# Kernel optimization log

Hardware: AMD Instinct MI355X
Metric: run time of the kernel (lower is better)

## Reference

```python
import jax, jax.numpy as jnp
import numpy as np

N_NODES = 20000
N_EDGES = 100000
WALK_LEN = 4
FEAT_DIM = 256
HID = 64
NUM_HEAD = 8
H_RNN = NUM_HEAD * HID  # 512
OUT_DIM = 16


def setup_inputs() -> dict:
    key = jax.random.key(0)
    ks = jax.random.split(key, 12)
    s = 0.05  # small init scale for numerical stability
    return {
        "x": jax.random.normal(ks[0], (N_NODES, FEAT_DIM), jnp.float32),
        "W_mlp": jax.random.normal(ks[1], (HID, FEAT_DIM), jnp.float32) * s,
        "b_mlp": jnp.zeros((HID,), jnp.float32),
        "W_ih": jax.random.normal(ks[2], (3 * H_RNN, HID), jnp.float32) * s,
        "W_hh": jax.random.normal(ks[3], (3 * H_RNN, H_RNN), jnp.float32) * s,
        "b_ih": jnp.zeros((3 * H_RNN,), jnp.float32),
        "b_hh": jnp.zeros((3 * H_RNN,), jnp.float32),
        "attn": jax.random.normal(ks[4], (1, NUM_HEAD, HID), jnp.float32) * s,
        "W_emb": jax.random.normal(ks[5], (HID, H_RNN), jnp.float32) * s,
        "b_emb": jnp.zeros((HID,), jnp.float32),
        "W_last": jax.random.normal(ks[6], (OUT_DIM, HID), jnp.float32) * s,
        "b_last": jnp.zeros((OUT_DIM,), jnp.float32),
        "edge_metapath_indices": jax.random.randint(ks[7], (N_EDGES, WALK_LEN), 0, N_NODES),
        "num_nodes": N_NODES,
    }


def reference(x, W_mlp, b_mlp, W_ih, W_hh, b_ih, b_hh, attn, W_emb, b_emb,
              W_last, b_last, edge_metapath_indices, num_nodes):
    # self channel: embedding = mlp(data.x)
    emb = x @ W_mlp.T + b_mlp                       # [N, hid]

    # rnn channel: gather per-metapath node embeddings
    edata = emb[edge_metapath_indices]              # [E, L, hid]
    E = edata.shape[0]
    h_rnn = W_hh.shape[1]

    # torch nn.GRU cell (gate order r, z, n), scan over path length
    def gru_step(h, x_t):
        xg = x_t @ W_ih.T + b_ih                    # [E, 3H]
        hg = h @ W_hh.T + b_hh                      # [E, 3H]
        xr, xz, xn = jnp.split(xg, 3, axis=-1)
        hr, hz, hn = jnp.split(hg, 3, axis=-1)
        r = jax.nn.sigmoid(xr + hr)
        z = jax.nn.sigmoid(xz + hz)
        n = jnp.tanh(xn + r * hn)
        return (1.0 - z) * n + z * h, None

    h0 = jnp.zeros((E, h_rnn), edata.dtype)
    hT, _ = jax.lax.scan(gru_step, h0, jnp.swapaxes(edata, 0, 1))  # [E, 8*hid]

    num_head, hid = attn.shape[1], attn.shape[2]
    eft = hT.reshape(E, num_head, hid)              # per-edge features

    # attention logits + leaky_relu(0.01)
    a = jnp.sum(eft * attn, axis=-1)                # [E, num_head]
    a = jnp.where(a > 0, a, 0.01 * a)

    # edge softmax grouped by destination node (indices[:, -1])
    dst = edge_metapath_indices[:, -1]
    m = jax.ops.segment_max(a, dst, num_segments=num_nodes)        # [N, H]
    ea = jnp.exp(a - m[dst])
    ssum = jax.ops.segment_sum(ea, dst, num_segments=num_nodes)    # [N, H]
    alpha = ea / ssum[dst]                          # [E, H]

    # message passing: scatter-sum of attention-weighted edge features
    ft = jax.ops.segment_sum(eft * alpha[:, :, None], dst,
                             num_segments=num_nodes)               # [N, H, hid]
    ret = ft.reshape(num_nodes, num_head * hid)
    rnn_emb = ret @ W_emb.T + b_emb                 # [N, hid]

    out = rnn_emb @ W_last.T + b_last               # [N, out_dim]
    return out
```

## Files before the change

### kernel.cpp

```cpp
#include <hip/hip_runtime.h>
#include <hip/hip_bf16.h>
#include <cstdint>

#define N_NODES 20000
#define N_EDGES 100000
#define WALK 4
#define FDIM 256
#define HID 64
#define NHEAD 8
#define HR 512
#define OUTD 16

typedef __attribute__((ext_vector_type(8))) short bf16x8;
typedef __attribute__((ext_vector_type(8))) unsigned short u16x8;
typedef __attribute__((ext_vector_type(4))) float f32x4;

__device__ __forceinline__ float b2f(unsigned short u){
  union{float f; unsigned u;} x; x.u = ((unsigned)u)<<16; return x.f;
}
__device__ __forceinline__ unsigned short f2b(float f){
  union{float f; unsigned u;} x; x.f = f;
  unsigned r = x.u + 0x7FFFu + ((x.u>>16)&1u);
  return (unsigned short)(r>>16);
}
__device__ __forceinline__ float sigmoidf_(float v){ return 1.0f/(1.0f+__expf(-v)); }
__device__ __forceinline__ float tanh_c(float v){
  v = fminf(fmaxf(v, -15.f), 15.f);
  const float t2 = __expf(2.0f*v);
  return (t2 - 1.0f) / (t2 + 1.0f);
}

__device__ __forceinline__ void gload16(const void* g, void* l){
  __builtin_amdgcn_global_load_lds(
      (const __attribute__((address_space(1))) void*)(g),
      (__attribute__((address_space(3))) void*)(l),
      16, 0, 0);
}

__device__ __forceinline__ f32x4 mfma16(bf16x8 a, bf16x8 b, f32x4 c){
  return __builtin_amdgcn_mfma_f32_16x16x32_bf16(a, b, c, 0, 0, 0);
}

__launch_bounds__(256)
__global__ void emb_kernel(const float* __restrict__ x,
                           const float* __restrict__ Wm,
                           const float* __restrict__ bm,
                           unsigned short* __restrict__ emb_bf)
{
  __shared__ float xs[4][FDIM];
  const int tid = threadIdx.x;
  const int node0 = blockIdx.x * 4;
  {
    const int row = tid >> 6;
    const int k4  = (tid & 63) * 4;
    *reinterpret_cast<float4*>(&xs[row][k4]) =
      *reinterpret_cast<const float4*>(&x[(size_t)(node0+row)*FDIM + k4]);
  }
  __syncthreads();
  const int nn = tid >> 6, c = tid & 63;
  float acc = bm[c];
  const float* wr = &Wm[c*FDIM];
  #pragma unroll 8
  for (int k=0;k<FDIM;k+=4){
    const float4 w = *reinterpret_cast<const float4*>(&wr[k]);
    acc += xs[nn][k]*w.x + xs[nn][k+1]*w.y + xs[nn][k+2]*w.z + xs[nn][k+3]*w.w;
  }
  emb_bf[(size_t)(node0+nn)*HID + c] = f2b(acc);
}

__launch_bounds__(256)
__global__ void prep_kernel(const float* __restrict__ Whh,
                            const float* __restrict__ Wih,
                            const float* __restrict__ Wemb,
                            unsigned short* __restrict__ WhhP,
                            unsigned short* __restrict__ WihP,
                            unsigned short* __restrict__ WembP)
{
  const int t = blockIdx.x*256 + threadIdx.x;
  if (t < 8*192*512){
    const int k = t & 511;
    const int r = (t >> 9) % 192;
    const int db = t / 98304;
    const int G = (r>>6)*HR + db*64 + (r&63);
    const int kg = k >> 6, kw = k & 63;
    const int c = kw >> 3, o = kw & 7;
    const int ksrc = (kg<<6) + (((c ^ (r&7)) << 3) | o);
    WhhP[t] = f2b(Whh[(size_t)G*HR + ksrc]);
  }
  if (t < 8*192*64){
    const int k = t & 63;
    const int r = (t >> 6) % 192;
    const int db = t / 12288;
    const int G = (r>>6)*HR + db*64 + (r&63);
    const int c = k >> 3, o = k & 7;
    const int ksrc = (((c ^ (r&7)) << 3) | o);
    WihP[t] = f2b(Wih[(size_t)G*HID + ksrc]);
  }
  if (t < 64*512){
    const int k = t & 511;
    const int o = t >> 9;
    const int kg = k >> 6, kw = k & 63;
    const int c = kw >> 3, off = kw & 7;
    const int ksrc = (kg<<6) + (((c ^ (o&7)) << 3) | off);
    WembP[t] = f2b(Wemb[(size_t)o*HR + ksrc]);
  }
}

__launch_bounds__(256)
__global__ void xg_kernel(const unsigned short* __restrict__ emb_bf,
                          const unsigned short* __restrict__ WihP,
                          const float* __restrict__ b_ih,
                          const float* __restrict__ b_hh,
                          unsigned short* __restrict__ xnP,
                          unsigned short* __restrict__ h1n)
{
  __shared__ __align__(16) unsigned short As[128*64];
  __shared__ __align__(16) unsigned short Bs[192*64];
  const int tid = threadIdx.x, lane = tid & 63, w = tid >> 6;
  const int tx = lane & 15, ty = lane >> 4;
  const int n0 = blockIdx.x * 128;
  const int db = blockIdx.y;

  #pragma unroll
  for (int j=0;j<4;++j){
    const int flat = j*256 + tid;
    const int row = flat >> 3, c = flat & 7;
    int n = n0 + row; if (n > N_NODES-1) n = N_NODES-1;
    gload16(emb_bf + ((size_t)n*HID + ((c ^ (row&7))<<3)), (char*)As + flat*16);
  }
  #pragma unroll
  for (int j=0;j<6;++j){
    const int flat = j*256 + tid;
    const int row = flat >> 3, c = flat & 7;
    gload16(WihP + ((size_t)(db*192 + row)*HID + c*8), (char*)Bs + flat*16);
  }
  __syncthreads();

  f32x4 acc[2][12];
  #pragma unroll
  for (int m=0;m<2;++m)
    #pragma unroll
    for (int f=0;f<12;++f) acc[m][f] = (f32x4)(0.f);

  auto readFrag = [&](const unsigned short* base, int row, int kk)->bf16x8{
    const int chunk = (kk<<2) + ty;
    return *reinterpret_cast<const bf16x8*>(
        reinterpret_cast<const char*>(base) + (row<<7) + ((chunk ^ (row&7))<<4));
  };
  #pragma unroll
  for (int kk=0; kk<2; ++kk){
    const bf16x8 a0 = readFrag(As, w*32 + tx, kk);
    const bf16x8 a1 = readFrag(As, w*32 + 16 + tx, kk);
    #pragma unroll
    for (int nf=0; nf<12; ++nf){
      const bf16x8 b = readFrag(Bs, nf*16 + tx, kk);
      acc[0][nf] = mfma16(a0, b, acc[0][nf]);
      acc[1][nf] = mfma16(a1, b, acc[1][nf]);
    }
  }

  #pragma unroll
  for (int m=0;m<2;++m){
    #pragma unroll
    for (int reg=0; reg<4; ++reg){
      const int row = w*32 + m*16 + ty*4 + reg;
      const int n = n0 + row;
      if (n < N_NODES){
        #pragma unroll
        for (int fr=0; fr<4; ++fr){
          const int d6 = fr*16 + tx;
          const int dG = db*64 + d6;
          const float xr = acc[m][fr][reg]   + b_ih[dG];
          const float xz = acc[m][4+fr][reg] + b_ih[HR+dG];
          const float xn = acc[m][8+fr][reg] + b_ih[2*HR+dG];
          xnP[((size_t)db*N_NODES + n)*64 + d6] = f2b(xn);
          const float r = sigmoidf_(xr + b_hh[dG]);
          const float z = sigmoidf_(xz + b_hh[HR+dG]);
          const float nn = tanh_c(xn + r*b_hh[2*HR+dG]);
          h1n[(size_t)n*HR + dG] = f2b((1.0f - z)*nn);
        }
      }
    }
  }
}

__launch_bounds__(256)
__global__ void hgn_kernel(const unsigned short* __restrict__ h1n,
                           const unsigned short* __restrict__ WhhP,
                           unsigned short* __restrict__ hgP)
{
  __shared__ __align__(16) unsigned short As[128*64];
  __shared__ __align__(16) unsigned short Bs[192*64];
  const int tid = threadIdx.x, lane = tid & 63, w = tid >> 6;
  const int tx = lane & 15, ty = lane >> 4;
  const int n0 = blockIdx.x * 128;
  const int db = blockIdx.y;

  f32x4 acc[2][12];
  #pragma unroll
  for (int m=0;m<2;++m)
    #pragma unroll
    for (int f=0;f<12;++f) acc[m][f] = (f32x4)(0.f);

  auto stageA = [&](int kt){
    #pragma unroll
    for (int j=0;j<4;++j){
      const int flat = j*256 + tid;
      const int row = flat >> 3, c = flat & 7;
      int n = n0 + row; if (n > N_NODES-1) n = N_NODES-1;
      gload16(h1n + ((size_t)n*HR + kt*64 + ((c ^ (row&7)) << 3)), (char*)As + flat*16);
    }
  };
  auto stageB = [&](int kt){
    #pragma unroll
    for (int j=0;j<6;++j){
      const int flat = j*256 + tid;
      const int row = flat >> 3, c = flat & 7;
      gload16(WhhP + ((size_t)(db*192 + row)*HR + kt*64 + c*8), (char*)Bs + flat*16);
    }
  };
  auto readFrag = [&](const unsigned short* base, int row, int kk)->bf16x8{
    const int chunk = (kk<<2) + ty;
    return *reinterpret_cast<const bf16x8*>(
        reinterpret_cast<const char*>(base) + (row<<7) + ((chunk ^ (row&7))<<4));
  };

  stageA(0); stageB(0);
  #pragma unroll
  for (int kt=0; kt<8; ++kt){
    __syncthreads();
    #pragma unroll
    for (int kk=0; kk<2; ++kk){
      const bf16x8 a0 = readFrag(As, w*32 + tx, kk);
      const bf16x8 a1 = readFrag(As, w*32 + 16 + tx, kk);
      #pragma unroll
      for (int nf=0; nf<12; ++nf){
        const bf16x8 b = readFrag(Bs, nf*16 + tx, kk);
        acc[0][nf] = mfma16(a0, b, acc[0][nf]);
        acc[1][nf] = mfma16(a1, b, acc[1][nf]);
      }
    }
    if (kt < 7){
      __syncthreads();
      stageA(kt+1); stageB(kt+1);
    }
  }

  #pragma unroll
  for (int m=0;m<2;++m){
    #pragma unroll
    for (int reg=0; reg<4; ++reg){
      const int row = w*32 + m*16 + ty*4 + reg;
      const int n = n0 + row;
      if (n < N_NODES){
        #pragma unroll
        for (int nf=0; nf<12; ++nf)
          hgP[((size_t)db*N_NODES + n)*192 + nf*16 + tx] = f2b(acc[m][nf][reg]);
      }
    }
  }
}

__launch_bounds__(256)
__global__ void step1x_kernel(const unsigned short* __restrict__ emb_bf,
                              const int* __restrict__ idx,
                              const unsigned short* __restrict__ h1n,
                              const unsigned short* __restrict__ hgP,
                              const unsigned short* __restrict__ xnP,
                              const unsigned short* __restrict__ WihP,
                              unsigned short* __restrict__ h_out,
                              const float* __restrict__ b_ih,
                              const float* __restrict__ b_hh)
{
  __shared__ __align__(16) unsigned short As[128*64];
  __shared__ __align__(16) unsigned short Bs[128*64];
  const int tid = threadIdx.x, lane = tid & 63, w = tid >> 6;
  const int tx = lane & 15, ty = lane >> 4;

  const int bid = blockIdx.x;
  const int sid = (bid & 7)*782 + (bid >> 3);
  const int et = sid >> 3;
  const int db = sid & 7;
  const int e0 = et * 128;

  #pragma unroll
  for (int j=0;j<4;++j){
    const int flat = j*256 + tid;
    const int row = flat >> 3, c = flat & 7;
    int e = e0 + row; if (e > N_EDGES-1) e = N_EDGES-1;
    const int n1 = idx[e*WALK + 1];
    gload16(emb_bf + ((size_t)n1*HID + ((c ^ (row&7)) << 3)), (char*)As + flat*16);
  }
  #pragma unroll
  for (int j=0;j<4;++j){
    const int flat = j*256 + tid;
    const int row = flat >> 3, c = flat & 7;
    gload16(WihP + ((size_t)(db*192 + row)*HID + c*8), (char*)Bs + flat*16);
  }
  __syncthreads();

  f32x4 acc[2][8];
  #pragma unroll
  for (int m=0;m<2;++m)
    #pragma unroll
    for (int f=0;f<8;++f) acc[m][f] = (f32x4)(0.f);

  auto readFrag = [&](const unsigned short* base, int row, int kk)->bf16x8{
    const int chunk = (kk<<2) + ty;
    return *reinterpret_cast<const bf16x8*>(
        reinterpret_cast<const char*>(base) + (row<<7) + ((chunk ^ (row&7))<<4));
  };
  #pragma unroll
  for (int kk=0; kk<2; ++kk){
    const bf16x8 a0 = readFrag(As, w*32 + tx, kk);
    const bf16x8 a1 = readFrag(As, w*32 + 16 + tx, kk);
    #pragma unroll
    for (int nf=0; nf<8; ++nf){
      const bf16x8 b = readFrag(Bs, nf*16 + tx, kk);
      acc[0][nf] = mfma16(a0, b, acc[0][nf]);
      acc[1][nf] = mfma16(a1, b, acc[1][nf]);
    }
  }

  float bir[4], biz[4], bhn[4];
  #pragma unroll
  for (int fr=0; fr<4; ++fr){
    const int dG = db*64 + fr*16 + tx;
    bir[fr] = b_ih[dG]      + b_hh[dG];
    biz[fr] = b_ih[HR+dG]   + b_hh[HR+dG];
    bhn[fr] = b_hh[2*HR+dG];
  }

  #pragma unroll
  for (int m=0;m<2;++m){
    #pragma unroll
    for (int reg=0; reg<4; ++reg){
      const int row = w*32 + m*16 + ty*4 + reg;
      const int e = e0 + row;
      if (e < N_EDGES){
        const int n0 = idx[e*WALK];
        const int n1 = idx[e*WALK + 1];
        const size_t hb = ((size_t)db*N_NODES + n0)*192;
        #pragma unroll
        for (int fr=0; fr<4; ++fr){
          const int d6 = fr*16 + tx;
          const int dG = db*64 + d6;
          const float hr = b2f(hgP[hb + d6]);
          const float hz = b2f(hgP[hb + 64 + d6]);
          const float hn = b2f(hgP[hb + 128 + d6]) + bhn[fr];
          const float xn = b2f(xnP[((size_t)db*N_NODES + n1)*64 + d6]);
          const float hold = b2f(h1n[(size_t)n0*HR + dG]);
          const float r  = sigmoidf_(acc[m][fr][reg]   + hr + bir[fr]);
          const float z  = sigmoidf_(acc[m][4+fr][reg] + hz + biz[fr]);
          const float nn = tanh_c(xn + r*hn);
          const float hv = (1.0f - z)*nn + z*hold;
          h_out[(size_t)e*HR + db*64 + (((d6>>3) ^ (e&7))<<3) + (d6&7)] = f2b(hv);
        }
      }
    }
  }
}

template<int STEP, bool SCORE>
__launch_bounds__(256)
__global__ void gru_mfma(const unsigned short* __restrict__ emb_bf,
                         const int* __restrict__ idx,
                         const unsigned short* __restrict__ h_in,
                         unsigned short* __restrict__ h_out,
                         const unsigned short* __restrict__ WhhP,
                         const unsigned short* __restrict__ WihP,
                         const unsigned short* __restrict__ xnP,
                         const float* __restrict__ b_ih,
                         const float* __restrict__ b_hh,
                         const float* __restrict__ attn,
                         float* __restrict__ a_buf,
                         unsigned int* __restrict__ mmax)
{
  __shared__ __align__(16) unsigned short As[128*64];
  __shared__ __align__(16) unsigned short Bs[192*64];

  const int tid = threadIdx.x, lane = tid & 63, w = tid >> 6;
  const int tx = lane & 15, ty = lane >> 4;

  const int bid = blockIdx.x;
  const int sid = (bid & 7)*782 + (bid >> 3);
  const int et = sid >> 3;
  const int db = sid & 7;
  const int e0 = et * 128;

  int eS[4], nX[4];
  #pragma unroll
  for (int j=0;j<4;++j){
    int e = e0 + ((j*256 + tid) >> 3);
    if (e > N_EDGES-1) e = N_EDGES-1;
    eS[j] = e;
    nX[j] = idx[e*WALK + STEP];
  }

  f32x4 acc[2][12];
  #pragma unroll
  for (int m=0;m<2;++m)
    #pragma unroll
    for (int f=0;f<12;++f) acc[m][f] = (f32x4)(0.f);

  auto stageA = [&](int kt){
    #pragma unroll
    for (int j=0;j<4;++j){
      const int flat = j*256 + tid;
      const int row = flat >> 3, c = flat & 7;
      const unsigned short* src;
      if (kt == 8){
        src = emb_bf + ((size_t)nX[j]*HID + ((c ^ (row&7)) << 3));
      } else {
        src = h_in + ((size_t)eS[j]*HR + kt*64 + c*8);
      }
      gload16(src, (char*)As + flat*16);
    }
  };
  auto stageB = [&](int kt){
    #pragma unroll
    for (int j=0;j<6;++j){
      const int flat = j*256 + tid;
      const int row = flat >> 3, c = flat & 7;
      const unsigned short* src = (kt < 8)
        ? WhhP + ((size_t)(db*192 + row)*HR + kt*64 + c*8)
        : WihP + ((size_t)(db*192 + row)*HID + c*8);
      gload16(src, (char*)Bs + flat*16);
    }
  };
  auto readFrag = [&](const unsigned short* base, int row, int kk)->bf16x8{
    const int chunk = (kk<<2) + ty;
    return *reinterpret_cast<const bf16x8*>(
        reinterpret_cast<const char*>(base) + (row<<7) + ((chunk ^ (row&7))<<4));
  };

  stageA(0); stageB(0);

  #pragma unroll
  for (int kt=0; kt<9; ++kt){
    __syncthreads();
    #pragma unroll
    for (int kk=0; kk<2; ++kk){
      const bf16x8 a0 = readFrag(As, w*32 + tx, kk);
      const bf16x8 a1 = readFrag(As, w*32 + 16 + tx, kk);
      #pragma unroll
      for (int nf=0; nf<12; ++nf){
        if (kt == 8 && nf >= 8) continue;
        const bf16x8 b = readFrag(Bs, nf*16 + tx, kk);
        acc[0][nf] = mfma16(a0, b, acc[0][nf]);
        acc[1][nf] = mfma16(a1, b, acc[1][nf]);
      }
    }
    if (kt < 8){
      __syncthreads();
      stageA(kt+1); stageB(kt+1);
    }
  }

  float bir[4], biz[4], bhn[4], atv[4];
  #pragma unroll
  for (int fr=0; fr<4; ++fr){
    const int dG = db*64 + fr*16 + tx;
    bir[fr] = b_ih[dG]      + b_hh[dG];
    biz[fr] = b_ih[HR+dG]   + b_hh[HR+dG];
    bhn[fr] = b_hh[2*HR+dG];
    atv[fr] = SCORE ? attn[dG] : 0.f;
  }

  #pragma unroll
  for (int m=0;m<2;++m){
    #pragma unroll
    for (int reg=0; reg<4; ++reg){
      const int row = w*32 + m*16 + ty*4 + reg;
      const int e = e0 + row;
      float sp = 0.f;
      if (e < N_EDGES){
        const int nodeS = idx[e*WALK + STEP];
        #pragma unroll
        for (int fr=0; fr<4; ++fr){
          const int d6 = fr*16 + tx;
          const float xn = b2f(xnP[((size_t)db*N_NODES + nodeS)*64 + d6]);
          const float hold = b2f(h_in[(size_t)e*HR + db*64 + (((d6>>3) ^ (e&7))<<3) + (d6&7)]);
          const float r  = sigmoidf_(acc[m][fr][reg]   + bir[fr]);
          const float z  = sigmoidf_(acc[m][4+fr][reg] + biz[fr]);
          const float nn = tanh_c(xn + r*(acc[m][8+fr][reg] + bhn[fr]));
          const float hv = (1.0f - z)*nn + z*hold;
          h_out[(size_t)e*HR + db*64 + (((d6>>3) ^ (e&7))<<3) + (d6&7)] = f2b(hv);
          if (SCORE) sp += hv * atv[fr];
        }
      }
      if (SCORE){
        sp += __shfl_xor(sp, 1);
        sp += __shfl_xor(sp, 2);
        sp += __shfl_xor(sp, 4);
        sp += __shfl_xor(sp, 8);
        if (tx == 0 && e < N_EDGES){
          const float a = sp > 0.f ? sp : 0.01f*sp;
          a_buf[e*NHEAD + db] = a;
          const int dst = idx[e*WALK + 3];
          union{float f; unsigned u;} xx; xx.f = a;
          const unsigned key = (xx.u & 0x80000000u) ? ~xx.u : (xx.u | 0x80000000u);
          atomicMax(&mmax[dst*NHEAD + db], key);
        }
      }
    }
  }
}

__launch_bounds__(256)
__global__ void ea_kernel(const int* __restrict__ idx,
                          float* __restrict__ a_buf,
                          const unsigned int* __restrict__ mmax,
                          float* __restrict__ ssum)
{
  const int flat = blockIdx.x*256 + threadIdx.x;
  const int e = flat >> 3, h = flat & 7;
  const int dst = idx[e*WALK + 3];
  const unsigned key = mmax[dst*NHEAD + h];
  union{float f; unsigned u;} x;
  x.u = (key & 0x80000000u) ? (key & 0x7FFFFFFFu) : ~key;
  const float ea = __expf(a_buf[flat] - x.f);
  a_buf[flat] = ea;
  atomicAdd(&ssum[dst*NHEAD + h], ea);
}

__launch_bounds__(256)
__global__ void z_kernel(const unsigned short* __restrict__ hT,
                         const int* __restrict__ idx,
                         const float* __restrict__ ea_buf,
                         const float* __restrict__ ssum,
                         const unsigned short* __restrict__ WembP,
                         float* __restrict__ zacc)
{
  __shared__ __align__(16) char zs[40960];
  char* Az = zs;
  char* Bz = zs + 32768;
  const int tid = threadIdx.x;
  const int lane = tid & 63;
  const int w = tid >> 6;
  const int e0 = blockIdx.x * 256;

  int ej[8], dstj[8];
  #pragma unroll
  for (int j=0;j<8;++j){
    int e = e0 + ((j*256 + tid) >> 3);
    if (e > N_EDGES-1) e = N_EDGES-1;
    ej[j] = e;
    dstj[j] = idx[e*WALK + 3];
  }

  f32x4 acc[4][4];
  #pragma unroll
  for (int m=0;m<4;++m)
    #pragma unroll
    for (int f=0;f<4;++f) acc[m][f] = (f32x4)(0.f);

  auto readFrag = [&](const char* base, int row, int kk)->bf16x8{
    const int chunk = (kk<<2) + (lane>>4);
    return *reinterpret_cast<const bf16x8*>(base + (row<<7) + ((chunk ^ (row&7))<<4));
  };

  #pragma unroll 1
  for (int kt=0; kt<8; ++kt){
    __syncthreads();
    #pragma unroll
    for (int j=0;j<8;++j){
      const int flat = j*256 + tid;
      const int e = ej[j];
      const u16x8 hv = *reinterpret_cast<const u16x8*>(hT + (size_t)e*HR + kt*64 + (flat&7)*8);
      const float al = ea_buf[e*NHEAD + kt] / ssum[dstj[j]*NHEAD + kt];
      union { bf16x8 v; unsigned short s[8]; } o;
      #pragma unroll
      for (int i=0;i<8;++i) o.s[i] = f2b(b2f(hv[i]) * al);
      *reinterpret_cast<bf16x8*>(Az + flat*16) = o.v;
    }
    #pragma unroll
    for (int j=0;j<2;++j){
      const int flat = j*256 + tid;
      const int row = flat >> 3, c = flat & 7;
      gload16(WembP + ((size_t)row*HR + kt*64 + c*8), Bz + ((j*256 + w*64)<<4));
    }
    __syncthreads();
    #pragma unroll
    for (int kk=0; kk<2; ++kk){
      bf16x8 a_[4];
      #pragma unroll
      for (int mf=0; mf<4; ++mf)
        a_[mf] = readFrag(Az, w*64 + mf*16 + (lane&15), kk);
      #pragma unroll
      for (int nf=0; nf<4; ++nf){
        const bf16x8 b_ = readFrag(Bz, nf*16 + (lane&15), kk);
        #pragma unroll
        for (int mf=0; mf<4; ++mf)
          acc[mf][nf] = mfma16(a_[mf], b_, acc[mf][nf]);
      }
    }
  }

  #pragma unroll
  for (int mf=0; mf<4; ++mf){
    #pragma unroll
    for (int reg=0; reg<4; ++reg){
      const int row = w*64 + mf*16 + ((lane>>4)<<2) + reg;
      const int e = e0 + row;
      if (e < N_EDGES){
        const int dst = idx[e*WALK + 3];
        #pragma unroll
        for (int nf=0; nf<4; ++nf){
          const int o = nf*16 + (lane&15);
          atomicAdd(&zacc[(size_t)dst*64 + o], acc[mf][nf][reg]);
        }
      }
    }
  }
}

__launch_bounds__(256)
__global__ void out2_kernel(const float* __restrict__ zacc,
                            const float* __restrict__ b_emb,
                            const float* __restrict__ W_last,
                            const float* __restrict__ b_last,
                            float* __restrict__ out)
{
  const int flat = blockIdx.x*256 + threadIdx.x;
  if (flat >= N_NODES*OUTD) return;
  const int n = flat >> 4, o = flat & 15;
  float s = b_last[o];
  const float* zr = &zacc[(size_t)n*64];
  const float* wl = &W_last[o*64];
  #pragma unroll
  for (int k=0;k<64;++k) s += (zr[k] + b_emb[k]) * wl[k];
  out[(size_t)n*OUTD + o] = s;
}

extern "C" void kernel_launch(void* const* d_in, const int* in_sizes, int n_in,
                              void* d_out, int out_size, void* d_ws, size_t ws_size,
                              hipStream_t stream)
{
  (void)in_sizes; (void)n_in; (void)out_size; (void)ws_size;
  const float* x      = (const float*)d_in[0];
  const float* W_mlp  = (const float*)d_in[1];
  const float* b_mlp  = (const float*)d_in[2];
  const float* W_ih   = (const float*)d_in[3];
  const float* W_hh   = (const float*)d_in[4];
  const float* b_ih   = (const float*)d_in[5];
  const float* b_hh   = (const float*)d_in[6];
  const float* attn   = (const float*)d_in[7];
  const float* W_emb  = (const float*)d_in[8];
  const float* b_emb  = (const float*)d_in[9];
  const float* W_last = (const float*)d_in[10];
  const float* b_last = (const float*)d_in[11];
  const int*   idx    = (const int*)d_in[12];
  float* out = (float*)d_out;

  char* ws = (char*)d_ws;
  unsigned short* WhhP   = (unsigned short*)(ws + 0);
  unsigned short* WihP   = (unsigned short*)(ws + 1572864);
  unsigned short* WembP  = (unsigned short*)(ws + 1769472);
  unsigned short* emb_bf = (unsigned short*)(ws + 1835008);
  unsigned short* xnP    = (unsigned short*)(ws + 4395008);
  float*          a_buf  = (float*)(ws + 24875008);
  unsigned int*   mmax   = (unsigned int*)(ws + 28075008);
  float*          ssum   = (float*)(ws + 28715008);
  float*          zacc   = (float*)(ws + 29355008);
  unsigned short* h_a    = (unsigned short*)(ws + 34475008);
  unsigned short* h_b    = (unsigned short*)(ws + 136875008);
  unsigned short* h1n    = h_b;
  unsigned short* hgP    = (unsigned short*)(ws + 157355008);

  (void)hipMemsetAsync(mmax, 0, 6400000, stream);

  prep_kernel<<<3072, 256, 0, stream>>>(W_hh, W_ih, W_emb, WhhP, WihP, WembP);
  emb_kernel<<<N_NODES/4, 256, 0, stream>>>(x, W_mlp, b_mlp, emb_bf);

  dim3 ngrid((N_NODES + 127)/128, 8);
  xg_kernel<<<ngrid, 256, 0, stream>>>(emb_bf, WihP, b_ih, b_hh, xnP, h1n);
  hgn_kernel<<<ngrid, 256, 0, stream>>>(h1n, WhhP, hgP);

  const int NWG = 782*8;
  step1x_kernel<<<NWG, 256, 0, stream>>>(emb_bf, idx, h1n, hgP, xnP, WihP, h_a, b_ih, b_hh);
  gru_mfma<2,false><<<NWG, 256, 0, stream>>>(emb_bf, idx, h_a, h_b, WhhP, WihP, xnP, b_ih, b_hh, attn, a_buf, mmax);
  gru_mfma<3,true ><<<NWG, 256, 0, stream>>>(emb_bf, idx, h_b, h_a, WhhP, WihP, xnP, b_ih, b_hh, attn, a_buf, mmax);

  ea_kernel<<<N_EDGES*NHEAD/256, 256, 0, stream>>>(idx, a_buf, mmax, ssum);
  z_kernel<<<391, 256, 0, stream>>>(h_a, idx, a_buf, ssum, WembP, zacc);
  out2_kernel<<<(N_NODES*OUTD+255)/256, 256, 0, stream>>>(zacc, b_emb, W_last, b_last, out);
}
```

Before: 1.170 ms.

## Load GRU A-fragments straight from global and halve z_kernel edge tile

In gru_mfma the activation operand (previous hidden state or gathered node embedding) is no longer staged through shared memory. Each lane now reads its bf16x8 fragments directly from global memory, reproducing the existing XOR swizzle, which removes the A-tile shared buffer and its store/read traffic. Separately, z_kernel processes 128 edges per block instead of 256 and launches twice as many blocks, using less shared memory and fewer accumulators per block to raise occupancy. The risks are less-coalesced, latency-exposed global reads inside the MFMA loop and more contended atomics and more weight reloads in z_kernel.

New measurement: 1.156 ms. Within noise of the previous version (-1.3%).

```diff
diff --git a/kernel.cpp b/kernel.cpp
--- a/kernel.cpp
+++ b/kernel.cpp
@@ -376,7 +376,6 @@
                          float* __restrict__ a_buf,
                          unsigned int* __restrict__ mmax)
 {
-  __shared__ __align__(16) unsigned short As[128*64];
   __shared__ __align__(16) unsigned short Bs[192*64];
 
   const int tid = threadIdx.x, lane = tid & 63, w = tid >> 6;
@@ -388,14 +387,10 @@
   const int db = sid & 7;
   const int e0 = et * 128;
 
-  int eS[4], nX[4];
-  #pragma unroll
-  for (int j=0;j<4;++j){
-    int e = e0 + ((j*256 + tid) >> 3);
-    if (e > N_EDGES-1) e = N_EDGES-1;
-    eS[j] = e;
-    nX[j] = idx[e*WALK + STEP];
-  }
+  int eA0 = e0 + w*32 + tx;      if (eA0 > N_EDGES-1) eA0 = N_EDGES-1;
+  int eA1 = e0 + w*32 + 16 + tx; if (eA1 > N_EDGES-1) eA1 = N_EDGES-1;
+  const int nX0 = idx[eA0*WALK + STEP];
+  const int nX1 = idx[eA1*WALK + STEP];
 
   f32x4 acc[2][12];
   #pragma unroll
@@ -403,20 +398,6 @@
     #pragma unroll
     for (int f=0;f<12;++f) acc[m][f] = (f32x4)(0.f);
 
-  auto stageA = [&](int kt){
-    #pragma unroll
-    for (int j=0;j<4;++j){
-      const int flat = j*256 + tid;
-      const int row = flat >> 3, c = flat & 7;
-      const unsigned short* src;
-      if (kt == 8){
-        src = emb_bf + ((size_t)nX[j]*HID + ((c ^ (row&7)) << 3));
-      } else {
-        src = h_in + ((size_t)eS[j]*HR + kt*64 + c*8);
-      }
-      gload16(src, (char*)As + flat*16);
-    }
-  };
   auto stageB = [&](int kt){
     #pragma unroll
     for (int j=0;j<6;++j){
@@ -428,32 +409,45 @@
       gload16(src, (char*)Bs + flat*16);
     }
   };
-  auto readFrag = [&](const unsigned short* base, int row, int kk)->bf16x8{
+  auto readB = [&](int row, int kk)->bf16x8{
     const int chunk = (kk<<2) + ty;
     return *reinterpret_cast<const bf16x8*>(
-        reinterpret_cast<const char*>(base) + (row<<7) + ((chunk ^ (row&7))<<4));
-  };
-
-  stageA(0); stageB(0);
+        reinterpret_cast<const char*>(Bs) + (row<<7) + ((chunk ^ (row&7))<<4));
+  };
+  auto loadA = [&](int e, int n, int kt, int kk)->bf16x8{
+    const unsigned short* p;
+    if (kt == 8){
+      p = emb_bf + ((size_t)n*HID + (((kk<<2)+ty) << 3));
+    } else {
+      p = h_in + ((size_t)e*HR + kt*64 + (((((kk<<2)+ty) ^ (e&7))) << 3));
+    }
+    return *reinterpret_cast<const bf16x8*>(p);
+  };
+
+  stageB(0);
 
   #pragma unroll
   for (int kt=0; kt<9; ++kt){
     __syncthreads();
+    const bf16x8 a00 = loadA(eA0, nX0, kt, 0);
+    const bf16x8 a10 = loadA(eA1, nX1, kt, 0);
+    const bf16x8 a01 = loadA(eA0, nX0, kt, 1);
+    const bf16x8 a11 = loadA(eA1, nX1, kt, 1);
     #pragma unroll
     for (int kk=0; kk<2; ++kk){
-      const bf16x8 a0 = readFrag(As, w*32 + tx, kk);
-      const bf16x8 a1 = readFrag(As, w*32 + 16 + tx, kk);
+      const bf16x8 a0 = kk ? a01 : a00;
+      const bf16x8 a1 = kk ? a11 : a10;
       #pragma unroll
       for (int nf=0; nf<12; ++nf){
         if (kt == 8 && nf >= 8) continue;
-        const bf16x8 b = readFrag(Bs, nf*16 + tx, kk);
+        const bf16x8 b = readB(nf*16 + tx, kk);
         acc[0][nf] = mfma16(a0, b, acc[0][nf]);
         acc[1][nf] = mfma16(a1, b, acc[1][nf]);
       }
     }
     if (kt < 8){
       __syncthreads();
-      stageA(kt+1); stageB(kt+1);
+      stageB(kt+1);
     }
   }
 
@@ -532,26 +526,26 @@
                          const unsigned short* __restrict__ WembP,
                          float* __restrict__ zacc)
 {
-  __shared__ __align__(16) char zs[40960];
+  __shared__ __align__(16) char zs[24576];
   char* Az = zs;
-  char* Bz = zs + 32768;
+  char* Bz = zs + 16384;
   const int tid = threadIdx.x;
   const int lane = tid & 63;
   const int w = tid >> 6;
-  const int e0 = blockIdx.x * 256;
-
-  int ej[8], dstj[8];
-  #pragma unroll
-  for (int j=0;j<8;++j){
+  const int e0 = blockIdx.x * 128;
+
+  int ej[4], dstj[4];
+  #pragma unroll
+  for (int j=0;j<4;++j){
     int e = e0 + ((j*256 + tid) >> 3);
     if (e > N_EDGES-1) e = N_EDGES-1;
     ej[j] = e;
     dstj[j] = idx[e*WALK + 3];
   }
 
-  f32x4 acc[4][4];
-  #pragma unroll
-  for (int m=0;m<4;++m)
+  f32x4 acc[2][4];
+  #pragma unroll
+  for (int m=0;m<2;++m)
     #pragma unroll
     for (int f=0;f<4;++f) acc[m][f] = (f32x4)(0.f);
 
@@ -564,7 +558,7 @@
   for (int kt=0; kt<8; ++kt){
     __syncthreads();
     #pragma unroll
-    for (int j=0;j<8;++j){
+    for (int j=0;j<4;++j){
       const int flat = j*256 + tid;
       const int e = ej[j];
       const u16x8 hv = *reinterpret_cast<const u16x8*>(hT + (size_t)e*HR + kt*64 + (flat&7)*8);
@@ -583,25 +577,25 @@
     __syncthreads();
     #pragma unroll
     for (int kk=0; kk<2; ++kk){
-      bf16x8 a_[4];
+      bf16x8 a_[2];
       #pragma unroll
-      for (int mf=0; mf<4; ++mf)
-        a_[mf] = readFrag(Az, w*64 + mf*16 + (lane&15), kk);
+      for (int mf=0; mf<2; ++mf)
+        a_[mf] = readFrag(Az, w*32 + mf*16 + (lane&15), kk);
       #pragma unroll
       for (int nf=0; nf<4; ++nf){
         const bf16x8 b_ = readFrag(Bz, nf*16 + (lane&15), kk);
         #pragma unroll
-        for (int mf=0; mf<4; ++mf)
+        for (int mf=0; mf<2; ++mf)
           acc[mf][nf] = mfma16(a_[mf], b_, acc[mf][nf]);
       }
     }
   }
 
   #pragma unroll
-  for (int mf=0; mf<4; ++mf){
+  for (int mf=0; mf<2; ++mf){
     #pragma unroll
     for (int reg=0; reg<4; ++reg){
-      const int row = w*64 + mf*16 + ((lane>>4)<<2) + reg;
+      const int row = w*32 + mf*16 + ((lane>>4)<<2) + reg;
       const int e = e0 + row;
       if (e < N_EDGES){
         const int dst = idx[e*WALK + 3];
@@ -683,6 +677,6 @@
   gru_mfma<3,true ><<<NWG, 256, 0, stream>>>(emb_bf, idx, h_b, h_a, WhhP, WihP, xnP, b_ih, b_hh, attn, a_buf, mmax);
 
   ea_kernel<<<N_EDGES*NHEAD/256, 256, 0, stream>>>(idx, a_buf, mmax, ssum);
-  z_kernel<<<391, 256, 0, stream>>>(h_a, idx, a_buf, ssum, WembP, zacc);
+  z_kernel<<<782, 256, 0, stream>>>(h_a, idx, a_buf, ssum, WembP, zacc);
   out2_kernel<<<(N_NODES*OUTD+255)/256, 256, 0, stream>>>(zacc, b_emb, W_last, b_last, out);
 }
```
